# Kernel tuning notes

Measured on AMD Instinct MI355X. Metric: run time of the kernel, lower is better.

## Reference

```python
import jax, jax.numpy as jnp
import numpy as np

D_MODEL = 1024
N_HEADS = 16
D_K = 64
CHUNK_LEN = 64
B, CHUNKS, NEIGHBORS, NEIGHBOR_LEN = 8, 32, 2, 128
SEQ = CHUNKS * CHUNK_LEN  # 2048
LN_EPS = 1e-5


def setup_inputs() -> dict:
    key = jax.random.key(0)
    ks = jax.random.split(key, 8)
    s = 0.02
    return {
        "h": jax.random.normal(ks[0], (B, SEQ, D_MODEL), dtype=jnp.float32),
        "e": jax.random.normal(ks[1], (B, CHUNKS, NEIGHBORS, NEIGHBOR_LEN, D_MODEL), dtype=jnp.float32),
        "Wq": jax.random.normal(ks[2], (D_MODEL, N_HEADS * D_K), dtype=jnp.float32) * s,
        "bq": jnp.zeros((N_HEADS * D_K,), dtype=jnp.float32),
        "Wk": jax.random.normal(ks[3], (D_MODEL, N_HEADS * D_K), dtype=jnp.float32) * s,
        "bk": jnp.zeros((N_HEADS * D_K,), dtype=jnp.float32),
        "Wv": jax.random.normal(ks[4], (D_MODEL, N_HEADS * D_K), dtype=jnp.float32) * s,
        "bv": jnp.zeros((N_HEADS * D_K,), dtype=jnp.float32),
        "gamma": jnp.ones((D_MODEL,), dtype=jnp.float32),
        "beta": jnp.zeros((D_MODEL,), dtype=jnp.float32),
        "Wo": jax.random.normal(ks[5], (N_HEADS * D_K, D_MODEL), dtype=jnp.float32) * s,
        "bo": jnp.zeros((D_MODEL,), dtype=jnp.float32),
    }


def _layer_norm(x, gamma, beta):
    mu = jnp.mean(x, axis=-1, keepdims=True)
    var = jnp.mean(jnp.square(x - mu), axis=-1, keepdims=True)
    return (x - mu) * jax.lax.rsqrt(var + LN_EPS) * gamma + beta


def reference(h, e, Wq, bq, Wk, bk, Wv, bv, gamma, beta, Wo, bo):
    batch, chunks, neighbors, neighbor_len, d_model = e.shape
    seq = h.shape[1]
    scale = 1.0 / np.sqrt(D_K)
    h_res = h

    # shift so each chunk attends only to completed retrieval chunks
    x = h[:, CHUNK_LEN - 1:]                      # [b, seq-(cl-1), d]
    x = _layer_norm(x, gamma, beta)
    pad = chunks * CHUNK_LEN - x.shape[1]
    x = jnp.pad(x, ((0, 0), (0, pad), (0, 0)))    # [b, chunks*cl, d]
    x = x.reshape(batch, chunks, CHUNK_LEN, d_model)

    q = (x @ Wq + bq).reshape(batch, chunks, CHUNK_LEN, N_HEADS, D_K)
    k = (e @ Wk + bk).reshape(batch, chunks, neighbors, neighbor_len, N_HEADS, D_K)
    v = (e @ Wv + bv).reshape(batch, chunks, neighbors, neighbor_len, N_HEADS, D_K)

    attn = jnp.einsum('bcihd,bcnjhd->bchinj', q, k) * scale   # [b,c,h,i,n,j]
    a_shape = attn.shape
    attn = jax.nn.softmax(attn.reshape(*a_shape[:4], -1), axis=-1).reshape(a_shape)

    o = jnp.einsum('bchinj,bcnjhd->bcihd', attn, v)           # [b,c,i,h,d]
    o = o.reshape(batch, chunks * CHUNK_LEN, N_HEADS * D_K)
    o = o @ Wo + bo
    # undo the shift: left-pad by chunk_len-1, truncate to seq
    o = jnp.pad(o, ((0, 0), (CHUNK_LEN - 1, 0), (0, 0)))[:, :seq]
    return o + h_res
```

## Files before the change

kernel.cpp:

```cpp
#include <hip/hip_runtime.h>
#include <hip/hip_bf16.h>

typedef __attribute__((ext_vector_type(8))) short bf16x8;
typedef __attribute__((ext_vector_type(4))) float f32x4;
typedef __attribute__((ext_vector_type(8))) unsigned short u16x8;

static __device__ __forceinline__ unsigned short f2bf(float f) {
  unsigned int u = __builtin_bit_cast(unsigned int, f);
  u += 0x7fffu + ((u >> 16) & 1u);
  return (unsigned short)(u >> 16);
}
static __device__ __forceinline__ unsigned int pk2(float lo, float hi) {
  return (unsigned int)f2bf(lo) | ((unsigned int)f2bf(hi) << 16);
}
static __device__ __forceinline__ void gload_lds16(const void* g, void* l) {
  __builtin_amdgcn_global_load_lds(
      (__attribute__((address_space(1))) void*)(g),
      (__attribute__((address_space(3))) void*)(l), 16, 0, 0);
}

__global__ __launch_bounds__(256) void cvt_bf16(const float* __restrict__ in,
                                                unsigned short* __restrict__ out,
                                                long n8) {
  const long stride = (long)gridDim.x * 256;
  for (long i = (long)blockIdx.x * 256 + threadIdx.x; i < n8; i += stride) {
    const float4 a = ((const float4*)in)[2 * i];
    const float4 b = ((const float4*)in)[2 * i + 1];
    uint4 w;
    w.x = pk2(a.x, a.y);
    w.y = pk2(a.z, a.w);
    w.z = pk2(b.x, b.y);
    w.w = pk2(b.z, b.w);
    ((uint4*)out)[i] = w;
  }
}

__global__ __launch_bounds__(256) void transpose_w(const float* __restrict__ W,
                                                   unsigned short* __restrict__ WT) {
  __shared__ float tile[64][65];
  const int bx = blockIdx.x;
  const int by = blockIdx.y;
  const int t = threadIdx.x;
  const int rr = t >> 6;
  const int cc = t & 63;
#pragma unroll
  for (int i = 0; i < 16; ++i) {
    int r = i * 4 + rr;
    tile[r][cc] = W[(size_t)(by * 64 + r) * 1024 + bx * 64 + cc];
  }
  __syncthreads();
#pragma unroll
  for (int i = 0; i < 16; ++i) {
    int n = i * 4 + rr;
    WT[(size_t)(bx * 64 + n) * 1024 + by * 64 + cc] = f2bf(tile[cc][n]);
  }
}

__global__ __launch_bounds__(256) void ln_kernel(const float* __restrict__ H,
                                                 const float* __restrict__ gamma,
                                                 const float* __restrict__ beta,
                                                 unsigned short* __restrict__ X) {
  const int row = blockIdx.x;
  const int b = row >> 11;
  const int t = row & 2047;
  const int tid = threadIdx.x;
  uint2* xo = (uint2*)(X + (size_t)row * 1024);
  if (t >= 1985) {
    uint2 z;
    z.x = 0;
    z.y = 0;
    xo[tid] = z;
    return;
  }
  const float4* hp = (const float4*)(H + (size_t)(b * 2048 + t + 63) * 1024);
  float4 v = hp[tid];
  float s = v.x + v.y + v.z + v.w;
  float q = v.x * v.x + v.y * v.y + v.z * v.z + v.w * v.w;
#pragma unroll
  for (int off = 32; off > 0; off >>= 1) {
    s += __shfl_down(s, off);
    q += __shfl_down(q, off);
  }
  __shared__ float red[8];
  const int lane = tid & 63, wid = tid >> 6;
  if (lane == 0) {
    red[wid] = s;
    red[4 + wid] = q;
  }
  __syncthreads();
  s = red[0] + red[1] + red[2] + red[3];
  q = red[4] + red[5] + red[6] + red[7];
  const float mu = s * (1.0f / 1024.0f);
  const float var = q * (1.0f / 1024.0f) - mu * mu;
  const float rs = rsqrtf(var + 1e-5f);
  const float4 g = ((const float4*)gamma)[tid];
  const float4 bb = ((const float4*)beta)[tid];
  uint2 w;
  w.x = pk2((v.x - mu) * rs * g.x + bb.x, (v.y - mu) * rs * g.y + bb.y);
  w.y = pk2((v.z - mu) * rs * g.z + bb.z, (v.w - mu) * rs * g.w + bb.w);
  xo[tid] = w;
}

__global__ __launch_bounds__(256) void fill_head(const float* __restrict__ H,
                                                 float* __restrict__ OUT) {
  const int idx = blockIdx.x * 256 + threadIdx.x;
  const int b = idx / 16128;
  const int rem = idx - b * 16128;
  const size_t off = (size_t)b * 524288 + rem;
  ((float4*)OUT)[off] = ((const float4*)H)[off];
}

#define BAR()                                 \
  {                                           \
    asm volatile("" ::: "memory");            \
    __builtin_amdgcn_s_barrier();             \
    __builtin_amdgcn_sched_barrier(0);        \
  }
#define SB0() __builtin_amdgcn_sched_barrier(0)
#define VMW2() asm volatile("s_waitcnt vmcnt(2)" ::: "memory")

#define LDA_(dst, mh, buf)                                                              \
  {                                                                                     \
    const char* base_ = (const char*)&lds[buf][wm][0];                                  \
    _Pragma("unroll") for (int mi = 0; mi < 4; ++mi) {                                  \
      const int r_ = (mh) * 64 + mi * 16 + lrow;                                        \
      dst[mi][0] = *(const bf16x8*)(base_ + r_ * 128 + (((0 + lk) ^ (r_ & 7)) * 16));   \
      dst[mi][1] = *(const bf16x8*)(base_ + r_ * 128 + (((4 + lk) ^ (r_ & 7)) * 16));   \
    }                                                                                   \
  }
#define LDB_(dst, nh, buf)                                                              \
  {                                                                                     \
    const char* base_ = (const char*)&lds[buf][2 + (wn >> 1)][0];                       \
    _Pragma("unroll") for (int ni = 0; ni < 2; ++ni) {                                  \
      const int r_ = (wn & 1) * 64 + (nh) * 32 + ni * 16 + lrow;                        \
      dst[ni][0] = *(const bf16x8*)(base_ + r_ * 128 + (((0 + lk) ^ (r_ & 7)) * 16));   \
      dst[ni][1] = *(const bf16x8*)(base_ + r_ * 128 + (((4 + lk) ^ (r_ & 7)) * 16));   \
    }                                                                                   \
  }
#define MMA_(mh, nh, A, B)                                                              \
  {                                                                                     \
    __builtin_amdgcn_s_setprio(1);                                                      \
    _Pragma("unroll") for (int mi = 0; mi < 4; ++mi)                                    \
        _Pragma("unroll") for (int ni = 0; ni < 2; ++ni) {                              \
      acc[(mh) * 4 + mi][(nh) * 2 + ni] = __builtin_amdgcn_mfma_f32_16x16x32_bf16(      \
          A[mi][0], B[ni][0], acc[(mh) * 4 + mi][(nh) * 2 + ni], 0, 0, 0);              \
      acc[(mh) * 4 + mi][(nh) * 2 + ni] = __builtin_amdgcn_mfma_f32_16x16x32_bf16(      \
          A[mi][1], B[ni][1], acc[(mh) * 4 + mi][(nh) * 2 + ni], 0, 0, 0);              \
    }                                                                                   \
    __builtin_amdgcn_s_setprio(0);                                                      \
  }

template <int MODE>
__global__ __launch_bounds__(512, 2) void gemm256(
    const unsigned short* __restrict__ A, const unsigned short* __restrict__ BT,
    const float* __restrict__ bias1, const float* __restrict__ bias2,
    unsigned short* __restrict__ C1, unsigned short* __restrict__ C2,
    const float* __restrict__ H, float* __restrict__ OUT) {
  __shared__ alignas(16) unsigned short lds[2][4][128 * 64];
  const int tid = threadIdx.x;
  const int lane = tid & 63;
  const int wid = tid >> 6;
  const int wm = wid >> 2, wn = wid & 3;
  const int lrow = lane & 15, lk = lane >> 4;

  const int nx = gridDim.x;
  const int orig = blockIdx.y * nx + blockIdx.x;
  const int cpx = (nx * gridDim.y) >> 3;
  const int swz = (orig & 7) * cpx + (orig >> 3);
  const int m0 = (swz / nx) * 256;
  const int n0 = (swz % nx) * 256;

  f32x4 acc[8][4] = {};
  bf16x8 af[4][2], ax[4][2], b0[2][2], b1[2][2];

  auto STAGE = [&](int slot, int kt) {
    const int buf = kt & 1;
    const int kc = kt < 16 ? kt : 15;
    const unsigned short* src = (slot < 2) ? A + (size_t)(m0 + slot * 128) * 1024
                                           : BT + (size_t)(n0 + (slot - 2) * 128) * 1024;
    unsigned short* dst = &lds[buf][slot][0];
#pragma unroll
    for (int l = 0; l < 2; ++l) {
      const int row = l * 64 + wid * 8 + (lane >> 3);
      const int ch = (lane & 7) ^ (row & 7);
      gload_lds16(src + (size_t)row * 1024 + kc * 64 + ch * 8,
                  (char*)dst + (l * 64 + wid * 8) * 128);
    }
  };

  STAGE(0, 0);
  STAGE(1, 0);
  STAGE(2, 0);
  STAGE(3, 0);
  STAGE(0, 1);
  VMW2();
  __builtin_amdgcn_s_barrier();

  for (int it = 0; it < 8; ++it) {
    const int t = 2 * it;
    LDA_(af, 0, 0);
    LDB_(b0, 0, 0);
    STAGE(1, t + 1);
    MMA_(0, 0, af, b0);
    SB0();
    LDB_(b1, 1, 0);
    LDA_(ax, 1, 0);
    BAR();
    STAGE(2, t + 1);
    MMA_(0, 1, af, b1);
    BAR();
    STAGE(3, t + 1);
    MMA_(1, 1, ax, b1);
    BAR();
    STAGE(0, t + 2);
    MMA_(1, 0, ax, b0);
    VMW2();
    BAR();
    LDA_(af, 0, 1);
    LDB_(b0, 0, 1);
    STAGE(1, t + 2);
    MMA_(0, 0, af, b0);
    SB0();
    LDB_(b1, 1, 1);
    LDA_(ax, 1, 1);
    BAR();
    STAGE(2, t + 2);
    MMA_(0, 1, af, b1);
    BAR();
    STAGE(3, t + 2);
    MMA_(1, 1, ax, b1);
    BAR();
    STAGE(0, t + 3);
    MMA_(1, 0, ax, b0);
    VMW2();
    BAR();
  }

  if (MODE == 0) {
    const float* bsel = (n0 < 1024) ? bias1 : bias2;
    const int cbase = (n0 < 1024) ? n0 : (n0 - 1024);
    unsigned short* Cp0 = (n0 < 1024) ? C1 : C2;
    float bsv[4];
#pragma unroll
    for (int N = 0; N < 4; ++N) bsv[N] = bsel[cbase + wn * 64 + N * 16 + lrow];
    float* arr = (float*)&lds[0][0][0];
    const int q4 = lane >> 4;
    __syncthreads();
#pragma unroll
    for (int p = 0; p < 4; ++p) {
      if (wm == (p >> 1)) {
#pragma unroll
        for (int mb = 0; mb < 4; ++mb) {
          const int M = (p & 1) * 4 + mb;
#pragma unroll
          for (int N = 0; N < 4; ++N) {
            const int cl = wn * 64 + N * 16 + lrow;
#pragma unroll
            for (int r = 0; r < 4; ++r) {
              arr[(mb * 16 + q4 * 4 + r) * 260 + cl] = acc[M][N][r] + bsv[N];
            }
          }
        }
      }
      __syncthreads();
#pragma unroll
      for (int k = 0; k < 4; ++k) {
        const int chunk = k * 512 + tid;
        const int row = chunk >> 5;
        const int c8 = chunk & 31;
        const float* s = arr + row * 260 + c8 * 8;
        float4 f0 = *(const float4*)(s);
        float4 f1 = *(const float4*)(s + 4);
        uint4 w;
        w.x = pk2(f0.x, f0.y);
        w.y = pk2(f0.z, f0.w);
        w.z = pk2(f1.x, f1.y);
        w.w = pk2(f1.z, f1.w);
        *(uint4*)(Cp0 + (size_t)(m0 + p * 64 + row) * 1024 + cbase + c8 * 8) = w;
      }
      __syncthreads();
    }
  } else {
    const int r0 = lane >> 4;
#pragma unroll
    for (int N = 0; N < 4; ++N) {
      const int col = n0 + wn * 64 + N * 16 + lrow;
      const float bsv = bias1[col];
#pragma unroll
      for (int M = 0; M < 8; ++M) {
        const int row = m0 + wm * 128 + M * 16 + r0 * 4;
#pragma unroll
        for (int r = 0; r < 4; ++r) {
          const int gr = row + r;
          if ((gr & 2047) < 1985) {
            const size_t idx = (size_t)(gr + 63) * 1024 + col;
            OUT[idx] = H[idx] + acc[M][N][r] + bsv;
          }
        }
      }
    }
  }
}

__global__ __launch_bounds__(256) void attn_kernel(
    const unsigned short* __restrict__ Q, const unsigned short* __restrict__ K,
    const unsigned short* __restrict__ V, unsigned short* __restrict__ O) {
  __shared__ alignas(16) unsigned short k_lds[256 * 64];
  __shared__ alignas(16) unsigned short v_t[64 * 256];
  const int w = ((blockIdx.x & 7) << 9) | (blockIdx.x >> 3);
  const int h = w & 15;
  const int bc = w >> 4;
  const int tid = threadIdx.x;
  const int lane = tid & 63;
  const int wid = tid >> 6;
  const size_t kv0 = (size_t)bc * 256 * 1024 + h * 64;

  bf16x8 qf[2];
  {
    const size_t qrow = (size_t)bc * 64 + wid * 16 + (lane & 15);
    const unsigned short* qp = Q + qrow * 1024 + h * 64 + (lane >> 4) * 8;
    qf[0] = *(const bf16x8*)(qp);
    qf[1] = *(const bf16x8*)(qp + 32);
  }
#pragma unroll
  for (int it = 0; it < 8; ++it) {
    const int j = it * 32 + (tid >> 3);
    const int c = tid & 7;
    const uint4 kv = *(const uint4*)(K + kv0 + (size_t)j * 1024 + c * 8);
    *(uint4*)((char*)k_lds + j * 128 + ((c ^ (j & 7)) * 16)) = kv;
  }
  {
    const int j = (tid >> 1) * 2;
    const int half = tid & 1;
#pragma unroll
    for (int cc2 = 0; cc2 < 4; ++cc2) {
      const int chunk = half * 4 + cc2;
      const int d0 = chunk * 8;
      u16x8 a = *(const u16x8*)(V + kv0 + (size_t)j * 1024 + d0);
      u16x8 b = *(const u16x8*)(V + kv0 + (size_t)(j + 1) * 1024 + d0);
#pragma unroll
      for (int dd = 0; dd < 8; ++dd) {
        const int d = d0 + dd;
        unsigned int p = (unsigned int)a[dd] | ((unsigned int)b[dd] << 16);
        *(unsigned int*)((char*)v_t + d * 512 + (((j >> 3) ^ (d & 7)) * 16) + ((j & 7) * 2)) = p;
      }
    }
  }
  __syncthreads();

  f32x4 accs[16] = {};
#pragma unroll
  for (int jt = 0; jt < 16; ++jt) {
#pragma unroll
    for (int ks = 0; ks < 2; ++ks) {
      const int r = jt * 16 + (lane & 15);
      bf16x8 kf = *(const bf16x8*)((const char*)k_lds + r * 128 +
                                   (((ks * 4 + (lane >> 4)) ^ (r & 7)) * 16));
      accs[jt] = __builtin_amdgcn_mfma_f32_16x16x32_bf16(qf[ks], kf, accs[jt], 0, 0, 0);
    }
  }
  __syncthreads();

  float inv_[4];
#pragma unroll
  for (int r = 0; r < 4; ++r) {
    float m = accs[0][r];
#pragma unroll
    for (int jt = 1; jt < 16; ++jt) m = fmaxf(m, accs[jt][r]);
#pragma unroll
    for (int mk = 1; mk < 16; mk <<= 1) m = fmaxf(m, __shfl_xor(m, mk));
    float s = 0.f;
#pragma unroll
    for (int jt = 0; jt < 16; ++jt) {
      float p = __expf((accs[jt][r] - m) * 0.125f);
      accs[jt][r] = p;
      s += p;
    }
#pragma unroll
    for (int mk = 1; mk < 16; mk <<= 1) s += __shfl_xor(s, mk);
    inv_[r] = 1.0f / s;
  }
  char* pbase = (char*)k_lds + wid * 8192;
  {
    const int jc = lane & 15;
    const int i0 = (lane >> 4) * 4;
#pragma unroll
    for (int jt = 0; jt < 16; ++jt) {
      const int j = jt * 16 + jc;
#pragma unroll
      for (int r = 0; r < 4; ++r) {
        const int i = i0 + r;
        *(unsigned short*)(pbase + i * 512 + (((j >> 3) ^ (i & 7)) * 16) + ((j & 7) * 2)) =
            f2bf(accs[jt][r] * inv_[r]);
      }
    }
  }
  __syncthreads();

  f32x4 acco[4] = {};
#pragma unroll
  for (int jb = 0; jb < 8; ++jb) {
    const int i = lane & 15;
    bf16x8 pf = *(const bf16x8*)(pbase + i * 512 + (((jb * 4 + (lane >> 4)) ^ (i & 7)) * 16));
#pragma unroll
    for (int ni = 0; ni < 4; ++ni) {
      const int d = ni * 16 + (lane & 15);
      bf16x8 vf = *(const bf16x8*)((const char*)v_t + d * 512 +
                                   (((jb * 4 + (lane >> 4)) ^ (d & 7)) * 16));
      acco[ni] = __builtin_amdgcn_mfma_f32_16x16x32_bf16(pf, vf, acco[ni], 0, 0, 0);
    }
  }
  {
    const size_t row0 = (size_t)bc * 64 + wid * 16 + (lane >> 4) * 4;
#pragma unroll
    for (int ni = 0; ni < 4; ++ni) {
      const int col = h * 64 + ni * 16 + (lane & 15);
#pragma unroll
      for (int r = 0; r < 4; ++r) {
        O[(row0 + r) * 1024 + col] = f2bf(acco[ni][r]);
      }
    }
  }
}

extern "C" void kernel_launch(void* const* d_in, const int* in_sizes, int n_in,
                              void* d_out, int out_size, void* d_ws, size_t ws_size,
                              hipStream_t stream) {
  const float* h = (const float*)d_in[0];
  const float* e = (const float*)d_in[1];
  const float* Wq = (const float*)d_in[2];
  const float* bq = (const float*)d_in[3];
  const float* Wk = (const float*)d_in[4];
  const float* bk = (const float*)d_in[5];
  const float* Wv = (const float*)d_in[6];
  const float* bv = (const float*)d_in[7];
  const float* gamma = (const float*)d_in[8];
  const float* beta = (const float*)d_in[9];
  const float* Wo = (const float*)d_in[10];
  const float* bo = (const float*)d_in[11];
  float* out = (float*)d_out;

  char* ws = (char*)d_ws;
  unsigned short* x = (unsigned short*)ws;
  unsigned short* q = (unsigned short*)(ws + (32ull << 20));
  unsigned short* kbuf = (unsigned short*)(ws + (64ull << 20));
  unsigned short* vbuf = (unsigned short*)(ws + (192ull << 20));
  unsigned short* ebf = (unsigned short*)(ws + (320ull << 20));
  unsigned short* wqT = (unsigned short*)(ws + (448ull << 20));
  unsigned short* wkvT = (unsigned short*)(ws + (450ull << 20));
  unsigned short* woT = (unsigned short*)(ws + (454ull << 20));
  unsigned short* o = x;

  dim3 tb(256);
  cvt_bf16<<<2048, tb, 0, stream>>>(e, ebf, 8388608L);
  transpose_w<<<dim3(16, 16), tb, 0, stream>>>(Wq, wqT);
  transpose_w<<<dim3(16, 16), tb, 0, stream>>>(Wk, wkvT);
  transpose_w<<<dim3(16, 16), tb, 0, stream>>>(Wv, wkvT + 1024 * 1024);
  transpose_w<<<dim3(16, 16), tb, 0, stream>>>(Wo, woT);
  ln_kernel<<<16384, tb, 0, stream>>>(h, gamma, beta, x);
  gemm256<0><<<dim3(4, 64), dim3(512), 0, stream>>>(x, wqT, bq, nullptr, q, nullptr,
                                                    nullptr, nullptr);
  gemm256<0><<<dim3(8, 256), dim3(512), 0, stream>>>(ebf, wkvT, bk, bv, kbuf, vbuf,
                                                     nullptr, nullptr);
  attn_kernel<<<4096, tb, 0, stream>>>(q, kbuf, vbuf, o);
  fill_head<<<504, tb, 0, stream>>>(h, out);
  gemm256<1><<<dim3(4, 64), dim3(512), 0, stream>>>(o, woT, bo, nullptr, nullptr, nullptr,
                                                    h, out);
}
```

Baseline: 623.1 us.

## Restructure GEMM K-loop prefetch schedule with paired stage loads and deeper vmcnt

Rewrites the double-buffered GEMM main loop as a TILE macro that issues the A1/B1 loads for the next k-tile together and the A0/B0 loads two tiles ahead, instead of spreading one slot load between each MMA block. The wait depth goes from vmcnt(2) to vmcnt(4), and a barrier now follows each LDS fragment read. The goal is to keep more global-to-LDS traffic in flight and rebalance it against the MFMA blocks. The trade-off is extra barriers per tile and a full vmcnt(0) drain before the epilogue.

```diff
diff --git a/kernel.cpp b/kernel.cpp
--- a/kernel.cpp
+++ b/kernel.cpp
@@ -116,8 +116,7 @@
     __builtin_amdgcn_s_barrier();             \
     __builtin_amdgcn_sched_barrier(0);        \
   }
-#define SB0() __builtin_amdgcn_sched_barrier(0)
-#define VMW2() asm volatile("s_waitcnt vmcnt(2)" ::: "memory")
+#define VMW4() asm volatile("s_waitcnt vmcnt(4)" ::: "memory")
 
 #define LDA_(dst, mh, buf)                                                              \
   {                                                                                     \
@@ -148,6 +147,33 @@
           A[mi][1], B[ni][1], acc[(mh) * 4 + mi][(nh) * 2 + ni], 0, 0, 0);              \
     }                                                                                   \
     __builtin_amdgcn_s_setprio(0);                                                      \
+  }
+#define TILE(tt, BUF)                         \
+  {                                           \
+                                      \
+    LDA_(af, 0, BUF);                         \
+    LDB_(b0, 0, BUF);                         \
+    STAGE(BUF ^ 1, 1, (tt) + 1);              \
+    STAGE(BUF ^ 1, 3, (tt) + 1);              \
+    BAR();                                    \
+    MMA_(0, 0, af, b0);                       \
+    BAR();                                    \
+                                      \
+    LDB_(b1, 1, BUF);                         \
+    BAR();                                    \
+    MMA_(0, 1, af, b1);                       \
+    BAR();                                    \
+                                      \
+    LDA_(ax, 1, BUF);                         \
+    BAR();                                    \
+    MMA_(1, 1, ax, b1);                       \
+    BAR();                                    \
+     \
+    STAGE(BUF, 0, (tt) + 2);                  \
+    STAGE(BUF, 2, (tt) + 2);                  \
+    MMA_(1, 0, ax, b0);                       \
+    VMW4();                                   \
+    BAR();                                    \
   }
 
 template <int MODE>
@@ -173,8 +199,7 @@
   f32x4 acc[8][4] = {};
   bf16x8 af[4][2], ax[4][2], b0[2][2], b1[2][2];
 
-  auto STAGE = [&](int slot, int kt) {
-    const int buf = kt & 1;
+  auto STAGE = [&](int buf, int slot, int kt) {
     const int kc = kt < 16 ? kt : 15;
     const unsigned short* src = (slot < 2) ? A + (size_t)(m0 + slot * 128) * 1024
                                            : BT + (size_t)(n0 + (slot - 2) * 128) * 1024;
@@ -188,53 +213,22 @@
     }
   };
 
-  STAGE(0, 0);
-  STAGE(1, 0);
-  STAGE(2, 0);
-  STAGE(3, 0);
-  STAGE(0, 1);
-  VMW2();
+  STAGE(0, 0, 0);
+  STAGE(0, 1, 0);
+  STAGE(0, 2, 0);
+  STAGE(0, 3, 0);
+  STAGE(1, 0, 1);
+  STAGE(1, 2, 1);
+  VMW4();
   __builtin_amdgcn_s_barrier();
 
   for (int it = 0; it < 8; ++it) {
     const int t = 2 * it;
-    LDA_(af, 0, 0);
-    LDB_(b0, 0, 0);
-    STAGE(1, t + 1);
-    MMA_(0, 0, af, b0);
-    SB0();
-    LDB_(b1, 1, 0);
-    LDA_(ax, 1, 0);
-    BAR();
-    STAGE(2, t + 1);
-    MMA_(0, 1, af, b1);
-    BAR();
-    STAGE(3, t + 1);
-    MMA_(1, 1, ax, b1);
-    BAR();
-    STAGE(0, t + 2);
-    MMA_(1, 0, ax, b0);
-    VMW2();
-    BAR();
-    LDA_(af, 0, 1);
-    LDB_(b0, 0, 1);
-    STAGE(1, t + 2);
-    MMA_(0, 0, af, b0);
-    SB0();
-    LDB_(b1, 1, 1);
-    LDA_(ax, 1, 1);
-    BAR();
-    STAGE(2, t + 2);
-    MMA_(0, 1, af, b1);
-    BAR();
-    STAGE(3, t + 2);
-    MMA_(1, 1, ax, b1);
-    BAR();
-    STAGE(0, t + 3);
-    MMA_(1, 0, ax, b0);
-    VMW2();
-    BAR();
-  }
+    TILE(t, 0);
+    TILE(t + 1, 1);
+  }
+  asm volatile("s_waitcnt vmcnt(0)" ::: "memory");
+  __syncthreads();
 
   if (MODE == 0) {
     const float* bsel = (n0 < 1024) ? bias1 : bias2;
@@ -245,7 +239,6 @@
     for (int N = 0; N < 4; ++N) bsv[N] = bsel[cbase + wn * 64 + N * 16 + lrow];
     float* arr = (float*)&lds[0][0][0];
     const int q4 = lane >> 4;
-    __syncthreads();
 #pragma unroll
     for (int p = 0; p < 4; ++p) {
       if (wm == (p >> 1)) {
```

Measured after the change: 589.8 us. -5.4%, faster.
